# Optimization experiments

Measured on AMD Instinct MI355X. Metric: run time of the kernel, lower is better.

## Reference

```python
import jax, jax.numpy as jnp
import numpy as np

N = 100000      # nodes
E = 1600000     # edges (avg degree 16)
F_IN = 128      # node feature dim
HID = 128       # conv1 out
EMB = 64        # conv2 out (embedding)
OUT = 40        # classes


def setup_inputs() -> dict:
    key = jax.random.key(0)
    ks = jax.random.split(key, 8)
    x = jax.random.normal(ks[0], (N, F_IN), dtype=jnp.float32)
    edge_index = jax.random.randint(ks[1], (2, E), 0, N, dtype=jnp.int64)

    def glorot(k, shape):
        lim = np.sqrt(6.0 / (shape[0] + shape[1])).astype(np.float32)
        return jax.random.uniform(k, shape, jnp.float32, -lim, lim)

    W1 = glorot(ks[2], (F_IN, HID)); b1 = jnp.zeros((HID,), jnp.float32)
    W2 = glorot(ks[3], (HID, EMB)); b2 = jnp.zeros((EMB,), jnp.float32)
    Wl = glorot(ks[4], (EMB, OUT)); bl = jnp.zeros((OUT,), jnp.float32)
    return {"x": x, "edge_index": edge_index,
            "W1": W1, "b1": b1, "W2": W2, "b2": b2, "Wl": Wl, "bl": bl}


def _gcn_conv(x, W, b, src, dst, norm, n):
    # GCNConv: linear transform first (smaller width earlier), then normalized
    # sparse aggregation: out_i = sum_{j->i} norm_e * (x_j W) + b
    h = x @ W
    out = jax.ops.segment_sum(h[src] * norm[:, None], dst, num_segments=n)
    return out + b


def reference(x, edge_index, W1, b1, W2, b2, Wl, bl):
    n = x.shape[0]
    loop = jnp.arange(n, dtype=edge_index.dtype)
    # add self loops (GCNConv default)
    src = jnp.concatenate([edge_index[0], loop])
    dst = jnp.concatenate([edge_index[1], loop])
    # symmetric degree normalization: D^{-1/2} (A+I) D^{-1/2}
    deg = jax.ops.segment_sum(jnp.ones_like(dst, x.dtype), dst, num_segments=n)
    dinv = jnp.where(deg > 0, jax.lax.rsqrt(deg), 0.0)
    norm = dinv[src] * dinv[dst]

    h = jax.nn.relu(_gcn_conv(x, W1, b1, src, dst, norm, n))
    # F.dropout(training=False) is identity in eval mode
    embedding = _gcn_conv(h, W2, b2, src, dst, norm, n)
    logits = embedding @ Wl + bl
    return jax.nn.log_softmax(logits, axis=1), embedding
```

## Files before the change

### kernel.cpp

```cpp
#include <hip/hip_runtime.h>
#include <math.h>

#define F_IN 128
#define HIDN 128
#define EMBD 64
#define OUTC 40

#define NBINS 1024
#define BIN_SHIFT 7
#define CSR_BLKS 256

__host__ __device__ static inline int imin(int a, int b) { return a < b ? a : b; }

typedef __attribute__((ext_vector_type(8))) short s16x8;
typedef __attribute__((ext_vector_type(4))) float f32x4;

__device__ __forceinline__ unsigned short f2bf(float f) {
    unsigned int u = __builtin_bit_cast(unsigned int, f);
    u = (u + 0x7FFFu + ((u >> 16) & 1u)) >> 16;
    return (unsigned short)u;
}
__device__ __forceinline__ float bflo(unsigned int v) {
    return __builtin_bit_cast(float, v << 16);
}
__device__ __forceinline__ float bfhi(unsigned int v) {
    return __builtin_bit_cast(float, v & 0xFFFF0000u);
}

__host__ __device__ static inline int csr_chunk(int E) {
    return (((E + CSR_BLKS - 1) / CSR_BLKS) + 3) & ~3;
}


__global__ __launch_bounds__(256) void coarse_hist_kernel(const int* __restrict__ dst,
                                                          int* __restrict__ bc, int E) {
    __shared__ int h[NBINS];
    for (int i = threadIdx.x; i < NBINS; i += 256) h[i] = 0;
    __syncthreads();
    const int chunk = csr_chunk(E);
    const int e0 = blockIdx.x * chunk;
    const int e1 = imin(e0 + chunk, E);
    for (int e = e0 + threadIdx.x; e < e1; e += 256)
        atomicAdd(&h[dst[e] >> BIN_SHIFT], 1);
    __syncthreads();
    for (int i = threadIdx.x; i < NBINS; i += 256)
        bc[blockIdx.x * NBINS + i] = h[i];
}

__global__ __launch_bounds__(64) void bin_prefix_kernel(int* __restrict__ bc,
                                                        int* __restrict__ bintot) {
    const int bin = blockIdx.x * 64 + threadIdx.x;
    int run = 0;
    for (int blk = 0; blk < CSR_BLKS; ++blk) {
        int v = bc[blk * NBINS + bin];
        bc[blk * NBINS + bin] = run;
        run += v;
    }
    bintot[bin] = run;
}

__global__ __launch_bounds__(1024) void bin_scan_kernel(const int* __restrict__ bintot,
                                                        int* __restrict__ cs) {
    __shared__ int s[NBINS];
    const int t = threadIdx.x;
    s[t] = bintot[t];
    __syncthreads();
    for (int off = 1; off < NBINS; off <<= 1) {
        int v = (t >= off) ? s[t - off] : 0;
        __syncthreads();
        s[t] += v;
        __syncthreads();
    }
    cs[t + 1] = s[t];
    if (t == 0) cs[0] = 0;
}

__global__ __launch_bounds__(256) void bin_scatter_kernel(const int* __restrict__ src,
                                                          const int* __restrict__ dst,
                                                          const int* __restrict__ bc,
                                                          const int* __restrict__ cs,
                                                          int* __restrict__ ebuf, int E) {
    __shared__ int cur[NBINS];
    for (int i = threadIdx.x; i < NBINS; i += 256)
        cur[i] = cs[i] + bc[blockIdx.x * NBINS + i];
    __syncthreads();
    const int chunk = csr_chunk(E);
    const int e0 = blockIdx.x * chunk;
    const int e1 = imin(e0 + chunk, E);
    int e = e0 + threadIdx.x * 4;
    for (; e + 3 < e1; e += 256 * 4) {
        int4 d = *(const int4*)(dst + e);
        int4 s = *(const int4*)(src + e);
        int p0 = atomicAdd(&cur[d.x >> BIN_SHIFT], 1);
        int p1 = atomicAdd(&cur[d.y >> BIN_SHIFT], 1);
        int p2 = atomicAdd(&cur[d.z >> BIN_SHIFT], 1);
        int p3 = atomicAdd(&cur[d.w >> BIN_SHIFT], 1);
        ebuf[p0] = (s.x << BIN_SHIFT) | (d.x & 127);
        ebuf[p1] = (s.y << BIN_SHIFT) | (d.y & 127);
        ebuf[p2] = (s.z << BIN_SHIFT) | (d.z & 127);
        ebuf[p3] = (s.w << BIN_SHIFT) | (d.w & 127);
    }
    for (; e < e1; ++e) {
        int d = dst[e];
        int pos = atomicAdd(&cur[d >> BIN_SHIFT], 1);
        ebuf[pos] = (src[e] << BIN_SHIFT) | (d & 127);
    }
}

__global__ __launch_bounds__(256) void fine_build_kernel(const int* __restrict__ ebuf,
                                                         const int* __restrict__ cs,
                                                         int* __restrict__ degi,
                                                         int* __restrict__ rowptr,
                                                         float* __restrict__ dinv,
                                                         int* __restrict__ col, int n) {
    __shared__ int h[128];
    __shared__ int fs[128];
    __shared__ int cur[128];
    const int b = blockIdx.x;
    const int node0 = b << BIN_SHIFT;
    const int t = threadIdx.x;
    if (t < 128) h[t] = 0;
    __syncthreads();
    const int e0 = cs[b], e1 = cs[b + 1];
    for (int e = e0 + t; e < e1; e += 256)
        atomicAdd(&h[ebuf[e] & 127], 1);
    __syncthreads();
    if (t < 128) fs[t] = h[t];
    __syncthreads();
    for (int off = 1; off < 128; off <<= 1) {
        int v = 0;
        if (t < 128 && t >= off) v = fs[t - off];
        __syncthreads();
        if (t < 128) fs[t] += v;
        __syncthreads();
    }
    if (t < 128) {
        int node = node0 + t;
        if (node < n) {
            int cnt = h[t];
            degi[node] = cnt;
            rowptr[node] = e0 + fs[t] - cnt;
            dinv[node] = rsqrtf((float)cnt + 1.0f);
        }
        cur[t] = 0;
    }
    __syncthreads();
    for (int e = e0 + t; e < e1; e += 256) {
        int p = ebuf[e];
        int li = p & 127;
        int loc = atomicAdd(&cur[li], 1);
        col[e0 + (fs[li] - h[li]) + loc] = p >> BIN_SHIFT;
    }
}

template <typename InT, int K, int M, int WM, int WN>
__global__ __launch_bounds__(256) void gemm_mfma_kernel(const InT* __restrict__ X,
                                                        const float* __restrict__ W,
                                                        const float* __restrict__ dinv,
                                                        unsigned short* __restrict__ Y,
                                                        int n, int ntiles) {
    constexpr int BM = 64;
    constexpr int WR = BM / WM;
    constexpr int WC = M / WN;
    constexpr int RF = WR / 16;
    constexpr int CF = WC / 16;
    constexpr int KS = K / 32;
    constexpr int ROWB = K * 2;
    constexpr int UPR = ROWB / 16;

    __shared__ char Xs[BM * ROWB];

    const int tid = threadIdx.x;
    const int lane = tid & 63;
    const int wid = tid >> 6;
    const int wrow = wid / WN;
    const int wcol = wid % WN;
    const int l15 = lane & 15;
    const int lhi = lane >> 4;

    s16x8 bfrag[CF][KS];
#pragma unroll
    for (int cf = 0; cf < CF; ++cf)
#pragma unroll
        for (int ks = 0; ks < KS; ++ks) {
            const int colg = wcol * WC + cf * 16 + l15;
            const int kbase = ks * 32 + lhi * 8;
            s16x8 b;
#pragma unroll
            for (int j = 0; j < 8; ++j)
                b[j] = (short)f2bf(W[(size_t)(kbase + j) * M + colg]);
            bfrag[cf][ks] = b;
        }

    for (int tile = blockIdx.x; tile < ntiles; tile += gridDim.x) {
        const int row0 = tile * BM;
        __syncthreads();
#pragma unroll
        for (int i = 0; i < (BM * UPR) / 256; ++i) {
            int g = i * 256 + tid;
            int r = g / UPR, u = g % UPR;
            int grow = row0 + r;
            int4 val = make_int4(0, 0, 0, 0);
            if (grow < n) {
                if constexpr (sizeof(InT) == 4) {
                    const float* src = (const float*)X + (size_t)grow * K + u * 8;
                    float4 f0 = *(const float4*)src;
                    float4 f1 = *(const float4*)(src + 4);
                    val.x = (int)(f2bf(f0.x) | ((unsigned int)f2bf(f0.y) << 16));
                    val.y = (int)(f2bf(f0.z) | ((unsigned int)f2bf(f0.w) << 16));
                    val.z = (int)(f2bf(f1.x) | ((unsigned int)f2bf(f1.y) << 16));
                    val.w = (int)(f2bf(f1.z) | ((unsigned int)f2bf(f1.w) << 16));
                } else {
                    val = *(const int4*)((const unsigned short*)X + (size_t)grow * K + u * 8);
                }
            }
            *(int4*)(Xs + r * ROWB + ((u ^ (r & 7)) * 16)) = val;
        }
        __syncthreads();

        f32x4 acc[RF][CF];
#pragma unroll
        for (int rf = 0; rf < RF; ++rf)
#pragma unroll
            for (int cf = 0; cf < CF; ++cf) acc[rf][cf] = (f32x4)(0.0f);
#pragma unroll
        for (int ks = 0; ks < KS; ++ks) {
            s16x8 afrag[RF];
#pragma unroll
            for (int rf = 0; rf < RF; ++rf) {
                int r = wrow * WR + rf * 16 + l15;
                int u = ks * 4 + lhi;
                afrag[rf] = *(const s16x8*)(Xs + r * ROWB + ((u ^ (r & 7)) * 16));
            }
#pragma unroll
            for (int rf = 0; rf < RF; ++rf)
#pragma unroll
                for (int cf = 0; cf < CF; ++cf)
                    acc[rf][cf] = __builtin_amdgcn_mfma_f32_16x16x32_bf16(
                        afrag[rf], bfrag[cf][ks], acc[rf][cf], 0, 0, 0);
        }

#pragma unroll
        for (int rf = 0; rf < RF; ++rf) {
#pragma unroll
            for (int reg = 0; reg < 4; ++reg) {
                int grow = row0 + wrow * WR + rf * 16 + lhi * 4 + reg;
                if (grow < n) {
                    float dv = dinv[grow];
#pragma unroll
                    for (int cf = 0; cf < CF; ++cf) {
                        int colg = wcol * WC + cf * 16 + l15;
                        Y[(size_t)grow * M + colg] = f2bf(acc[rf][cf][reg] * dv);
                    }
                }
            }
        }
    }
}

__global__ __launch_bounds__(256) void gather_gemm_kernel(
    const unsigned short* __restrict__ Hs1, const int* __restrict__ rowptr,
    const int* __restrict__ degi, const int* __restrict__ col,
    const float* __restrict__ dinv, const float* __restrict__ b1,
    const float* __restrict__ W2, unsigned short* __restrict__ Hs2, int n) {
    __shared__ char h_tile[16 * 256];

    const int tid = threadIdx.x;
    const int lane = tid & 63;
    const int wv = tid >> 6;
    const int sub = lane & 15;
    const int grp = lane >> 4;
    const int node0 = blockIdx.x * 16;
    const int local = wv * 4 + grp;
    const int node = node0 + local;
    const int foff = sub * 8;

    s16x8 bfrag[4];
#pragma unroll
    for (int ks = 0; ks < 4; ++ks) {
        const int colg = wv * 16 + sub;
        const int kbase = ks * 32 + grp * 8;
        s16x8 bb;
#pragma unroll
        for (int j = 0; j < 8; ++j)
            bb[j] = (short)f2bf(W2[(size_t)(kbase + j) * EMBD + colg]);
        bfrag[ks] = bb;
    }

    if (node < n) {
        const int start = rowptr[node];
        const int cnt = degi[node];
        const float dvn = dinv[node];
        float acc[8];
        {
            int4 v = *(const int4*)(Hs1 + (size_t)node * HIDN + foff);
#pragma unroll
            for (int q = 0; q < 4; ++q) {
                unsigned int w = ((const unsigned int*)&v)[q];
                acc[2 * q] = bflo(w);
                acc[2 * q + 1] = bfhi(w);
            }
        }
        int m0 = imin(cnt, 16);
        int sv = (sub < m0) ? col[start + sub] : 0;
        for (int base = 0; base < cnt; base += 16) {
            int m = imin(cnt - base, 16);
            int svn = 0;
            int nb = base + 16;
            if (nb < cnt) {
                int mn = imin(cnt - nb, 16);
                svn = (sub < mn) ? col[start + nb + sub] : 0;
            }
            int k = 0;
            for (; k + 8 <= m; k += 8) {
                int4 a[8];
#pragma unroll
                for (int j = 0; j < 8; ++j) {
                    int s = __shfl(sv, k + j, 16);
                    a[j] = *(const int4*)(Hs1 + (size_t)s * HIDN + foff);
                }
#pragma unroll
                for (int j = 0; j < 8; ++j)
#pragma unroll
                    for (int q = 0; q < 4; ++q) {
                        unsigned int w = ((const unsigned int*)&a[j])[q];
                        acc[2 * q] += bflo(w);
                        acc[2 * q + 1] += bfhi(w);
                    }
            }
            for (; k + 2 <= m; k += 2) {
                int s0 = __shfl(sv, k, 16);
                int s1 = __shfl(sv, k + 1, 16);
                int4 a0 = *(const int4*)(Hs1 + (size_t)s0 * HIDN + foff);
                int4 a1 = *(const int4*)(Hs1 + (size_t)s1 * HIDN + foff);
#pragma unroll
                for (int q = 0; q < 4; ++q) {
                    unsigned int w0 = ((const unsigned int*)&a0)[q];
                    unsigned int w1 = ((const unsigned int*)&a1)[q];
                    acc[2 * q] += bflo(w0);
                    acc[2 * q + 1] += bfhi(w0);
                    acc[2 * q] += bflo(w1);
                    acc[2 * q + 1] += bfhi(w1);
                }
            }
            for (; k < m; ++k) {
                int s = __shfl(sv, k, 16);
                int4 a = *(const int4*)(Hs1 + (size_t)s * HIDN + foff);
#pragma unroll
                for (int q = 0; q < 4; ++q) {
                    unsigned int w = ((const unsigned int*)&a)[q];
                    acc[2 * q] += bflo(w);
                    acc[2 * q + 1] += bfhi(w);
                }
            }
            sv = svn;
        }
        float4 bv0 = *(const float4*)(b1 + foff);
        float4 bv1 = *(const float4*)(b1 + foff + 4);
        float o[8];
        o[0] = fmaxf(dvn * acc[0] + bv0.x, 0.f);
        o[1] = fmaxf(dvn * acc[1] + bv0.y, 0.f);
        o[2] = fmaxf(dvn * acc[2] + bv0.z, 0.f);
        o[3] = fmaxf(dvn * acc[3] + bv0.w, 0.f);
        o[4] = fmaxf(dvn * acc[4] + bv1.x, 0.f);
        o[5] = fmaxf(dvn * acc[5] + bv1.y, 0.f);
        o[6] = fmaxf(dvn * acc[6] + bv1.z, 0.f);
        o[7] = fmaxf(dvn * acc[7] + bv1.w, 0.f);
        int4 p;
        ((unsigned int*)&p)[0] = f2bf(o[0]) | ((unsigned int)f2bf(o[1]) << 16);
        ((unsigned int*)&p)[1] = f2bf(o[2]) | ((unsigned int)f2bf(o[3]) << 16);
        ((unsigned int*)&p)[2] = f2bf(o[4]) | ((unsigned int)f2bf(o[5]) << 16);
        ((unsigned int*)&p)[3] = f2bf(o[6]) | ((unsigned int)f2bf(o[7]) << 16);
        *(int4*)(h_tile + local * 256 + ((sub ^ (local & 7)) * 16)) = p;
    }
    __syncthreads();

    f32x4 acc2 = (f32x4)(0.0f);
#pragma unroll
    for (int ks = 0; ks < 4; ++ks) {
        int r = sub;
        int u = ks * 4 + grp;
        s16x8 af = *(const s16x8*)(h_tile + r * 256 + ((u ^ (r & 7)) * 16));
        acc2 = __builtin_amdgcn_mfma_f32_16x16x32_bf16(af, bfrag[ks], acc2, 0, 0, 0);
    }
#pragma unroll
    for (int reg = 0; reg < 4; ++reg) {
        int row = grp * 4 + reg;
        int nd = node0 + row;
        if (nd < n)
            Hs2[(size_t)nd * EMBD + wv * 16 + sub] = f2bf(acc2[reg] * dinv[nd]);
    }
}

template <int F, bool RELU, bool OBF>
__global__ __launch_bounds__(256) void gather_kernel(const unsigned short* __restrict__ Hs,
                                                     const int* __restrict__ rowptr,
                                                     const int* __restrict__ degi,
                                                     const int* __restrict__ col,
                                                     const float* __restrict__ dinv,
                                                     const float* __restrict__ b,
                                                     float* __restrict__ outf,
                                                     unsigned short* __restrict__ outb,
                                                     int n) {
    constexpr int LPF = F / 8;
    constexpr int NPW = 64 / LPF;
    const int lane = threadIdx.x & 63;
    const int wv = threadIdx.x >> 6;
    const int sub = lane & (LPF - 1);
    const int grp = lane / LPF;
    const int node = (blockIdx.x * 4 + wv) * NPW + grp;
    if (node >= n) return;
    const int start = rowptr[node];
    const int cnt = degi[node];
    const int foff = sub * 8;
    const float dvn = dinv[node];

    float acc[8];
    {
        int4 v = *(const int4*)(Hs + (size_t)node * F + foff);
#pragma unroll
        for (int q = 0; q < 4; ++q) {
            unsigned int w = ((const unsigned int*)&v)[q];
            acc[2 * q] = bflo(w);
            acc[2 * q + 1] = bfhi(w);
        }
    }

    int m0 = imin(cnt, LPF);
    int sv = (sub < m0) ? col[start + sub] : 0;
    for (int base = 0; base < cnt; base += LPF) {
        int m = imin(cnt - base, LPF);
        int svn = 0;
        int nb = base + LPF;
        if (nb < cnt) {
            int mn = imin(cnt - nb, LPF);
            svn = (sub < mn) ? col[start + nb + sub] : 0;
        }
        int k = 0;
        for (; k + 8 <= m; k += 8) {
            int4 a[8];
#pragma unroll
            for (int j = 0; j < 8; ++j) {
                int s = __shfl(sv, k + j, LPF);
                a[j] = *(const int4*)(Hs + (size_t)s * F + foff);
            }
#pragma unroll
            for (int j = 0; j < 8; ++j)
#pragma unroll
                for (int q = 0; q < 4; ++q) {
                    unsigned int w = ((const unsigned int*)&a[j])[q];
                    acc[2 * q] += bflo(w);
                    acc[2 * q + 1] += bfhi(w);
                }
        }
        for (; k < m; ++k) {
            int s = __shfl(sv, k, LPF);
            int4 a = *(const int4*)(Hs + (size_t)s * F + foff);
#pragma unroll
            for (int q = 0; q < 4; ++q) {
                unsigned int w = ((const unsigned int*)&a)[q];
                acc[2 * q] += bflo(w);
                acc[2 * q + 1] += bfhi(w);
            }
        }
        sv = svn;
    }

    float4 bv0 = *(const float4*)(b + foff);
    float4 bv1 = *(const float4*)(b + foff + 4);
    float o[8];
    o[0] = dvn * acc[0] + bv0.x; o[1] = dvn * acc[1] + bv0.y;
    o[2] = dvn * acc[2] + bv0.z; o[3] = dvn * acc[3] + bv0.w;
    o[4] = dvn * acc[4] + bv1.x; o[5] = dvn * acc[5] + bv1.y;
    o[6] = dvn * acc[6] + bv1.z; o[7] = dvn * acc[7] + bv1.w;
    if (RELU) {
#pragma unroll
        for (int j = 0; j < 8; ++j) o[j] = fmaxf(o[j], 0.0f);
    }
    if constexpr (OBF) {
        int4 p;
        ((unsigned int*)&p)[0] = f2bf(o[0]) | ((unsigned int)f2bf(o[1]) << 16);
        ((unsigned int*)&p)[1] = f2bf(o[2]) | ((unsigned int)f2bf(o[3]) << 16);
        ((unsigned int*)&p)[2] = f2bf(o[4]) | ((unsigned int)f2bf(o[5]) << 16);
        ((unsigned int*)&p)[3] = f2bf(o[6]) | ((unsigned int)f2bf(o[7]) << 16);
        *(int4*)(outb + (size_t)node * F + foff) = p;
    } else {
        float4 w0 = make_float4(o[0], o[1], o[2], o[3]);
        float4 w1 = make_float4(o[4], o[5], o[6], o[7]);
        *(float4*)(outf + (size_t)node * F + foff) = w0;
        *(float4*)(outf + (size_t)node * F + foff + 4) = w1;
    }
}

#define LSM_STRIDE 257
__global__ __launch_bounds__(256) void logits_lsm_kernel(const float* __restrict__ emb,
                                                         const float* __restrict__ Wl,
                                                         const float* __restrict__ bl,
                                                         float* __restrict__ out, int n) {
    __shared__ float Sbuf[EMBD * LSM_STRIDE];
    __shared__ float Wls[EMBD * OUTC];
    __shared__ float bls[OUTC];
    const int tid = threadIdx.x;
    const int node0 = blockIdx.x * 256;
    for (int i = tid; i < EMBD * OUTC; i += 256) Wls[i] = Wl[i];
    if (tid < OUTC) bls[tid] = bl[tid];

    const size_t base = (size_t)node0 * EMBD;
    const size_t total_elems = (size_t)n * EMBD;
    for (int it = 0; it < 16; ++it) {
        int idx = (tid + it * 256) * 4;
        int r = idx / EMBD, f = idx % EMBD;
        float4 v = make_float4(0.f, 0.f, 0.f, 0.f);
        if (base + idx + 3 < total_elems) v = *(const float4*)(emb + base + idx);
        Sbuf[(f + 0) * LSM_STRIDE + r] = v.x;
        Sbuf[(f + 1) * LSM_STRIDE + r] = v.y;
        Sbuf[(f + 2) * LSM_STRIDE + r] = v.z;
        Sbuf[(f + 3) * LSM_STRIDE + r] = v.w;
    }
    __syncthreads();

    float logit[OUTC];
#pragma unroll
    for (int o = 0; o < OUTC; ++o) logit[o] = bls[o];
    for (int f = 0; f < EMBD; ++f) {
        float ef = Sbuf[f * LSM_STRIDE + tid];
#pragma unroll
        for (int o = 0; o < OUTC; ++o) logit[o] = fmaf(ef, Wls[f * OUTC + o], logit[o]);
    }
    float mx = -INFINITY;
#pragma unroll
    for (int o = 0; o < OUTC; ++o) mx = fmaxf(mx, logit[o]);
    float s = 0.0f;
#pragma unroll
    for (int o = 0; o < OUTC; ++o) s += expf(logit[o] - mx);
    float lse = mx + logf(s);
    __syncthreads();
#pragma unroll
    for (int o = 0; o < OUTC; ++o) Sbuf[o * LSM_STRIDE + tid] = logit[o] - lse;
    __syncthreads();

    const size_t obase = (size_t)node0 * OUTC;
    const size_t ototal = (size_t)n * OUTC;
    for (int idx = tid; idx < 256 * OUTC; idx += 256) {
        size_t g = obase + idx;
        if (g < ototal) out[g] = Sbuf[(idx % OUTC) * LSM_STRIDE + (idx / OUTC)];
    }
}

extern "C" void kernel_launch(void* const* d_in, const int* in_sizes, int n_in,
                              void* d_out, int out_size, void* d_ws, size_t ws_size,
                              hipStream_t stream) {
    const float* x  = (const float*)d_in[0];
    const int*   ei = (const int*)d_in[1];
    const float* W1 = (const float*)d_in[2];
    const float* b1 = (const float*)d_in[3];
    const float* W2 = (const float*)d_in[4];
    const float* b2 = (const float*)d_in[5];
    const float* Wl = (const float*)d_in[6];
    const float* bl = (const float*)d_in[7];

    const int N = in_sizes[0] / F_IN;
    const int E = in_sizes[1] / 2;
    const int* srcp = ei;
    const int* dstp = ei + E;

    float* out = (float*)d_out;
    float* lsm = out;
    float* emb = out + (size_t)N * OUTC;

    float* ws    = (float*)d_ws;
    float* dinv  = ws;
    int*   degi  = (int*)(ws + N);
    int*   rowptr= degi + N;
    int*   cs    = rowptr + N;
    int*   bintot= cs + 1056;
    int*   bc    = bintot + NBINS;
    int*   col   = bc + CSR_BLKS * NBINS;
    int*   ebuf  = col + E;
    unsigned short* Hs1 = (unsigned short*)(ebuf + E);
    unsigned short* Hs2 = Hs1 + (size_t)N * HIDN;

    const int B = 256;
    const int ntiles = (N + 63) / 64;

    coarse_hist_kernel<<<CSR_BLKS, B, 0, stream>>>(dstp, bc, E);
    bin_prefix_kernel<<<NBINS / 64, 64, 0, stream>>>(bc, bintot);
    bin_scan_kernel<<<1, 1024, 0, stream>>>(bintot, cs);
    bin_scatter_kernel<<<CSR_BLKS, B, 0, stream>>>(srcp, dstp, bc, cs, ebuf, E);
    fine_build_kernel<<<(N + 127) / 128, B, 0, stream>>>(ebuf, cs, degi, rowptr, dinv, col, N);

    gemm_mfma_kernel<float, F_IN, HIDN, 2, 2><<<784, B, 0, stream>>>(x, W1, dinv, Hs1, N, ntiles);

    gather_gemm_kernel<<<(N + 15) / 16, B, 0, stream>>>(
        Hs1, rowptr, degi, col, dinv, b1, W2, Hs2, N);

    gather_kernel<EMBD, false, false><<<(N + 31) / 32, B, 0, stream>>>(
        Hs2, rowptr, degi, col, dinv, b2, emb, nullptr, N);

    logits_lsm_kernel<<<(N + 255) / 256, B, 0, stream>>>(emb, Wl, bl, lsm, N);
}
```

Baseline: 214.6 us.

## Fuse second aggregation with logits/log-softmax via MFMA and precompute weight fragments

```diff
diff --git a/kernel.cpp b/kernel.cpp
--- a/kernel.cpp
+++ b/kernel.cpp
@@ -31,6 +31,40 @@
     return (((E + CSR_BLKS - 1) / CSR_BLKS) + 3) & ~3;
 }
 
+__global__ __launch_bounds__(256) void prep_frags_kernel(
+    const float* __restrict__ W1, const float* __restrict__ W2,
+    const float* __restrict__ Wl, unsigned short* __restrict__ W1f,
+    unsigned short* __restrict__ W2f, unsigned short* __restrict__ Wlf) {
+    int s = blockIdx.x * 256 + threadIdx.x;
+    if (s < 2048) {
+        int lane = s & 63, r = s >> 6;
+        int ks = r & 3, cf = (r >> 2) & 3, wcol = r >> 4;
+        int c = wcol * 64 + cf * 16 + (lane & 15);
+        int kb = ks * 32 + (lane >> 4) * 8;
+        unsigned short* d = W1f + s * 8;
+#pragma unroll
+        for (int j = 0; j < 8; ++j) d[j] = f2bf(W1[(size_t)(kb + j) * HIDN + c]);
+    } else if (s < 3072) {
+        int q = s - 2048;
+        int lane = q & 63, r = q >> 6;
+        int ks = r & 3, wv = r >> 2;
+        int c = wv * 16 + (lane & 15);
+        int kb = ks * 32 + (lane >> 4) * 8;
+        unsigned short* d = W2f + q * 8;
+#pragma unroll
+        for (int j = 0; j < 8; ++j) d[j] = f2bf(W2[(size_t)(kb + j) * EMBD + c]);
+    } else if (s < 3456) {
+        int q = s - 3072;
+        int lane = q & 63, r = q >> 6;
+        int ks = r & 1, ct = r >> 1;
+        int c = ct * 16 + (lane & 15);
+        int kb = ks * 32 + (lane >> 4) * 8;
+        unsigned short* d = Wlf + q * 8;
+#pragma unroll
+        for (int j = 0; j < 8; ++j)
+            d[j] = (c < OUTC) ? f2bf(Wl[(size_t)(kb + j) * OUTC + c]) : (unsigned short)0;
+    }
+}
 
 __global__ __launch_bounds__(256) void coarse_hist_kernel(const int* __restrict__ dst,
                                                           int* __restrict__ bc, int E) {
@@ -155,7 +189,7 @@
 
 template <typename InT, int K, int M, int WM, int WN>
 __global__ __launch_bounds__(256) void gemm_mfma_kernel(const InT* __restrict__ X,
-                                                        const float* __restrict__ W,
+                                                        const unsigned short* __restrict__ Wfrag,
                                                         const float* __restrict__ dinv,
                                                         unsigned short* __restrict__ Y,
                                                         int n, int ntiles) {
@@ -182,15 +216,9 @@
 #pragma unroll
     for (int cf = 0; cf < CF; ++cf)
 #pragma unroll
-        for (int ks = 0; ks < KS; ++ks) {
-            const int colg = wcol * WC + cf * 16 + l15;
-            const int kbase = ks * 32 + lhi * 8;
-            s16x8 b;
-#pragma unroll
-            for (int j = 0; j < 8; ++j)
-                b[j] = (short)f2bf(W[(size_t)(kbase + j) * M + colg]);
-            bfrag[cf][ks] = b;
-        }
+        for (int ks = 0; ks < KS; ++ks)
+            bfrag[cf][ks] = *(const s16x8*)(Wfrag +
+                (size_t)(((wcol * CF + cf) * KS + ks) * 64 + lane) * 8);
 
     for (int tile = blockIdx.x; tile < ntiles; tile += gridDim.x) {
         const int row0 = tile * BM;
@@ -262,7 +290,7 @@
     const unsigned short* __restrict__ Hs1, const int* __restrict__ rowptr,
     const int* __restrict__ degi, const int* __restrict__ col,
     const float* __restrict__ dinv, const float* __restrict__ b1,
-    const float* __restrict__ W2, unsigned short* __restrict__ Hs2, int n) {
+    const unsigned short* __restrict__ W2f, unsigned short* __restrict__ Hs2, int n) {
     __shared__ char h_tile[16 * 256];
 
     const int tid = threadIdx.x;
@@ -277,15 +305,8 @@
 
     s16x8 bfrag[4];
 #pragma unroll
-    for (int ks = 0; ks < 4; ++ks) {
-        const int colg = wv * 16 + sub;
-        const int kbase = ks * 32 + grp * 8;
-        s16x8 bb;
-#pragma unroll
-        for (int j = 0; j < 8; ++j)
-            bb[j] = (short)f2bf(W2[(size_t)(kbase + j) * EMBD + colg]);
-        bfrag[ks] = bb;
-    }
+    for (int ks = 0; ks < 4; ++ks)
+        bfrag[ks] = *(const s16x8*)(W2f + (size_t)((wv * 4 + ks) * 64 + lane) * 8);
 
     if (node < n) {
         const int start = rowptr[node];
@@ -392,158 +413,141 @@
     }
 }
 
-template <int F, bool RELU, bool OBF>
-__global__ __launch_bounds__(256) void gather_kernel(const unsigned short* __restrict__ Hs,
-                                                     const int* __restrict__ rowptr,
-                                                     const int* __restrict__ degi,
-                                                     const int* __restrict__ col,
-                                                     const float* __restrict__ dinv,
-                                                     const float* __restrict__ b,
-                                                     float* __restrict__ outf,
-                                                     unsigned short* __restrict__ outb,
-                                                     int n) {
-    constexpr int LPF = F / 8;
-    constexpr int NPW = 64 / LPF;
-    const int lane = threadIdx.x & 63;
-    const int wv = threadIdx.x >> 6;
-    const int sub = lane & (LPF - 1);
-    const int grp = lane / LPF;
-    const int node = (blockIdx.x * 4 + wv) * NPW + grp;
-    if (node >= n) return;
-    const int start = rowptr[node];
-    const int cnt = degi[node];
+__global__ __launch_bounds__(256) void gather2_lsm_kernel(
+    const unsigned short* __restrict__ Hs, const int* __restrict__ rowptr,
+    const int* __restrict__ degi, const int* __restrict__ col,
+    const float* __restrict__ dinv, const float* __restrict__ b2,
+    const unsigned short* __restrict__ Wlf, const float* __restrict__ bl,
+    float* __restrict__ emb, float* __restrict__ lsm, int n) {
+    __shared__ char h_tile[32 * 128];
+    __shared__ float lg[32][49];
+    __shared__ float bls[OUTC];
+
+    const int tid = threadIdx.x;
+    if (tid < OUTC) bls[tid] = bl[tid];
+    const int lane = tid & 63;
+    const int wv = tid >> 6;
+    const int sub = lane & 7;
+    const int grp = lane >> 3;
+    const int local = wv * 8 + grp;
+    const int node0 = blockIdx.x * 32;
+    const int node = node0 + local;
     const int foff = sub * 8;
-    const float dvn = dinv[node];
-
-    float acc[8];
-    {
-        int4 v = *(const int4*)(Hs + (size_t)node * F + foff);
-#pragma unroll
-        for (int q = 0; q < 4; ++q) {
-            unsigned int w = ((const unsigned int*)&v)[q];
-            acc[2 * q] = bflo(w);
-            acc[2 * q + 1] = bfhi(w);
-        }
-    }
-
-    int m0 = imin(cnt, LPF);
-    int sv = (sub < m0) ? col[start + sub] : 0;
-    for (int base = 0; base < cnt; base += LPF) {
-        int m = imin(cnt - base, LPF);
-        int svn = 0;
-        int nb = base + LPF;
-        if (nb < cnt) {
-            int mn = imin(cnt - nb, LPF);
-            svn = (sub < mn) ? col[start + nb + sub] : 0;
-        }
-        int k = 0;
-        for (; k + 8 <= m; k += 8) {
-            int4 a[8];
-#pragma unroll
-            for (int j = 0; j < 8; ++j) {
-                int s = __shfl(sv, k + j, LPF);
-                a[j] = *(const int4*)(Hs + (size_t)s * F + foff);
-            }
-#pragma unroll
-            for (int j = 0; j < 8; ++j)
+
+    if (node < n) {
+        const int start = rowptr[node];
+        const int cnt = degi[node];
+        const float dvn = dinv[node];
+        float acc[8];
+        {
+            int4 v = *(const int4*)(Hs + (size_t)node * EMBD + foff);
+#pragma unroll
+            for (int q = 0; q < 4; ++q) {
+                unsigned int w = ((const unsigned int*)&v)[q];
+                acc[2 * q] = bflo(w);
+                acc[2 * q + 1] = bfhi(w);
+            }
+        }
+        int m0 = imin(cnt, 8);
+        int sv = (sub < m0) ? col[start + sub] : 0;
+        for (int base = 0; base < cnt; base += 8) {
+            int m = imin(cnt - base, 8);
+            int svn = 0;
+            int nb = base + 8;
+            if (nb < cnt) {
+                int mn = imin(cnt - nb, 8);
+                svn = (sub < mn) ? col[start + nb + sub] : 0;
+            }
+            int k = 0;
+            for (; k + 8 <= m; k += 8) {
+                int4 a[8];
+#pragma unroll
+                for (int j = 0; j < 8; ++j) {
+                    int s = __shfl(sv, k + j, 8);
+                    a[j] = *(const int4*)(Hs + (size_t)s * EMBD + foff);
+                }
+#pragma unroll
+                for (int j = 0; j < 8; ++j)
+#pragma unroll
+                    for (int q = 0; q < 4; ++q) {
+                        unsigned int w = ((const unsigned int*)&a[j])[q];
+                        acc[2 * q] += bflo(w);
+                        acc[2 * q + 1] += bfhi(w);
+                    }
+            }
+            for (; k < m; ++k) {
+                int s = __shfl(sv, k, 8);
+                int4 a = *(const int4*)(Hs + (size_t)s * EMBD + foff);
 #pragma unroll
                 for (int q = 0; q < 4; ++q) {
-                    unsigned int w = ((const unsigned int*)&a[j])[q];
+                    unsigned int w = ((const unsigned int*)&a)[q];
                     acc[2 * q] += bflo(w);
                     acc[2 * q + 1] += bfhi(w);
                 }
-        }
-        for (; k < m; ++k) {
-            int s = __shfl(sv, k, LPF);
-            int4 a = *(const int4*)(Hs + (size_t)s * F + foff);
-#pragma unroll
-            for (int q = 0; q < 4; ++q) {
-                unsigned int w = ((const unsigned int*)&a)[q];
-                acc[2 * q] += bflo(w);
-                acc[2 * q + 1] += bfhi(w);
-            }
-        }
-        sv = svn;
-    }
-
-    float4 bv0 = *(const float4*)(b + foff);
-    float4 bv1 = *(const float4*)(b + foff + 4);
-    float o[8];
-    o[0] = dvn * acc[0] + bv0.x; o[1] = dvn * acc[1] + bv0.y;
-    o[2] = dvn * acc[2] + bv0.z; o[3] = dvn * acc[3] + bv0.w;
-    o[4] = dvn * acc[4] + bv1.x; o[5] = dvn * acc[5] + bv1.y;
-    o[6] = dvn * acc[6] + bv1.z; o[7] = dvn * acc[7] + bv1.w;
-    if (RELU) {
-#pragma unroll
-        for (int j = 0; j < 8; ++j) o[j] = fmaxf(o[j], 0.0f);
-    }
-    if constexpr (OBF) {
+            }
+            sv = svn;
+        }
+
+        float4 bv0 = *(const float4*)(b2 + foff);
+        float4 bv1 = *(const float4*)(b2 + foff + 4);
+        float o[8];
+        o[0] = dvn * acc[0] + bv0.x; o[1] = dvn * acc[1] + bv0.y;
+        o[2] = dvn * acc[2] + bv0.z; o[3] = dvn * acc[3] + bv0.w;
+        o[4] = dvn * acc[4] + bv1.x; o[5] = dvn * acc[5] + bv1.y;
+        o[6] = dvn * acc[6] + bv1.z; o[7] = dvn * acc[7] + bv1.w;
+        *(float4*)(emb + (size_t)node * EMBD + foff) = make_float4(o[0], o[1], o[2], o[3]);
+        *(float4*)(emb + (size_t)node * EMBD + foff + 4) = make_float4(o[4], o[5], o[6], o[7]);
         int4 p;
         ((unsigned int*)&p)[0] = f2bf(o[0]) | ((unsigned int)f2bf(o[1]) << 16);
         ((unsigned int*)&p)[1] = f2bf(o[2]) | ((unsigned int)f2bf(o[3]) << 16);
         ((unsigned int*)&p)[2] = f2bf(o[4]) | ((unsigned int)f2bf(o[5]) << 16);
         ((unsigned int*)&p)[3] = f2bf(o[6]) | ((unsigned int)f2bf(o[7]) << 16);
-        *(int4*)(outb + (size_t)node * F + foff) = p;
-    } else {
-        float4 w0 = make_float4(o[0], o[1], o[2], o[3]);
-        float4 w1 = make_float4(o[4], o[5], o[6], o[7]);
-        *(float4*)(outf + (size_t)node * F + foff) = w0;
-        *(float4*)(outf + (size_t)node * F + foff + 4) = w1;
-    }
-}
-
-#define LSM_STRIDE 257
-__global__ __launch_bounds__(256) void logits_lsm_kernel(const float* __restrict__ emb,
-                                                         const float* __restrict__ Wl,
-                                                         const float* __restrict__ bl,
-                                                         float* __restrict__ out, int n) {
-    __shared__ float Sbuf[EMBD * LSM_STRIDE];
-    __shared__ float Wls[EMBD * OUTC];
-    __shared__ float bls[OUTC];
-    const int tid = threadIdx.x;
-    const int node0 = blockIdx.x * 256;
-    for (int i = tid; i < EMBD * OUTC; i += 256) Wls[i] = Wl[i];
-    if (tid < OUTC) bls[tid] = bl[tid];
-
-    const size_t base = (size_t)node0 * EMBD;
-    const size_t total_elems = (size_t)n * EMBD;
-    for (int it = 0; it < 16; ++it) {
-        int idx = (tid + it * 256) * 4;
-        int r = idx / EMBD, f = idx % EMBD;
-        float4 v = make_float4(0.f, 0.f, 0.f, 0.f);
-        if (base + idx + 3 < total_elems) v = *(const float4*)(emb + base + idx);
-        Sbuf[(f + 0) * LSM_STRIDE + r] = v.x;
-        Sbuf[(f + 1) * LSM_STRIDE + r] = v.y;
-        Sbuf[(f + 2) * LSM_STRIDE + r] = v.z;
-        Sbuf[(f + 3) * LSM_STRIDE + r] = v.w;
-    }
-    __syncthreads();
-
-    float logit[OUTC];
-#pragma unroll
-    for (int o = 0; o < OUTC; ++o) logit[o] = bls[o];
-    for (int f = 0; f < EMBD; ++f) {
-        float ef = Sbuf[f * LSM_STRIDE + tid];
-#pragma unroll
-        for (int o = 0; o < OUTC; ++o) logit[o] = fmaf(ef, Wls[f * OUTC + o], logit[o]);
-    }
-    float mx = -INFINITY;
-#pragma unroll
-    for (int o = 0; o < OUTC; ++o) mx = fmaxf(mx, logit[o]);
-    float s = 0.0f;
-#pragma unroll
-    for (int o = 0; o < OUTC; ++o) s += expf(logit[o] - mx);
-    float lse = mx + logf(s);
-    __syncthreads();
-#pragma unroll
-    for (int o = 0; o < OUTC; ++o) Sbuf[o * LSM_STRIDE + tid] = logit[o] - lse;
-    __syncthreads();
-
-    const size_t obase = (size_t)node0 * OUTC;
-    const size_t ototal = (size_t)n * OUTC;
-    for (int idx = tid; idx < 256 * OUTC; idx += 256) {
-        size_t g = obase + idx;
-        if (g < ototal) out[g] = Sbuf[(idx % OUTC) * LSM_STRIDE + (idx / OUTC)];
+        *(int4*)(h_tile + local * 128 + ((sub ^ (local & 7)) * 16)) = p;
+    }
+    __syncthreads();
+
+    const int l15 = lane & 15;
+    const int lhi = lane >> 4;
+#pragma unroll
+    for (int it = 0; it < 2; ++it) {
+        int t = wv + it * 4;
+        if (t < 6) {
+            int rt = t & 1, ct = t >> 1;
+            f32x4 accl = (f32x4)(0.0f);
+#pragma unroll
+            for (int ks = 0; ks < 2; ++ks) {
+                int r = rt * 16 + l15;
+                int u = ks * 4 + lhi;
+                s16x8 af = *(const s16x8*)(h_tile + r * 128 + ((u ^ (r & 7)) * 16));
+                s16x8 bf = *(const s16x8*)(Wlf + (size_t)((ct * 2 + ks) * 64 + lane) * 8);
+                accl = __builtin_amdgcn_mfma_f32_16x16x32_bf16(af, bf, accl, 0, 0, 0);
+            }
+#pragma unroll
+            for (int reg = 0; reg < 4; ++reg)
+                lg[rt * 16 + lhi * 4 + reg][ct * 16 + l15] = accl[reg];
+        }
+    }
+    __syncthreads();
+
+    if (tid < 32) {
+        int nd = node0 + tid;
+        if (nd < n) {
+            float logit[OUTC];
+            float mx = -INFINITY;
+#pragma unroll
+            for (int c = 0; c < OUTC; ++c) {
+                float v = lg[tid][c] + bls[c];
+                logit[c] = v;
+                mx = fmaxf(mx, v);
+            }
+            float ss = 0.0f;
+#pragma unroll
+            for (int c = 0; c < OUTC; ++c) ss += expf(logit[c] - mx);
+            float lse = mx + logf(ss);
+            float* op = lsm + (size_t)nd * OUTC;
+#pragma unroll
+            for (int c = 0; c < OUTC; ++c) op[c] = logit[c] - lse;
+        }
     }
 }
 
@@ -575,13 +579,18 @@
     int*   cs    = rowptr + N;
     int*   bintot= cs + 1056;
     int*   bc    = bintot + NBINS;
-    int*   col   = bc + CSR_BLKS * NBINS;
+    unsigned short* W1f = (unsigned short*)(bc + CSR_BLKS * NBINS);
+    unsigned short* W2f = W1f + 16384;
+    unsigned short* Wlf = W2f + 8192;
+    int*   col   = (int*)(Wlf + 3072);
     int*   ebuf  = col + E;
     unsigned short* Hs1 = (unsigned short*)(ebuf + E);
     unsigned short* Hs2 = Hs1 + (size_t)N * HIDN;
 
     const int B = 256;
     const int ntiles = (N + 63) / 64;
+
+    prep_frags_kernel<<<14, B, 0, stream>>>(W1, W2, Wl, W1f, W2f, Wlf);
 
     coarse_hist_kernel<<<CSR_BLKS, B, 0, stream>>>(dstp, bc, E);
     bin_prefix_kernel<<<NBINS / 64, 64, 0, stream>>>(bc, bintot);
@@ -589,13 +598,11 @@
     bin_scatter_kernel<<<CSR_BLKS, B, 0, stream>>>(srcp, dstp, bc, cs, ebuf, E);
     fine_build_kernel<<<(N + 127) / 128, B, 0, stream>>>(ebuf, cs, degi, rowptr, dinv, col, N);
 
-    gemm_mfma_kernel<float, F_IN, HIDN, 2, 2><<<784, B, 0, stream>>>(x, W1, dinv, Hs1, N, ntiles);
+    gemm_mfma_kernel<float, F_IN, HIDN, 2, 2><<<784, B, 0, stream>>>(x, W1f, dinv, Hs1, N, ntiles);
 
     gather_gemm_kernel<<<(N + 15) / 16, B, 0, stream>>>(
-        Hs1, rowptr, degi, col, dinv, b1, W2, Hs2, N);
-
-    gather_kernel<EMBD, false, false><<<(N + 31) / 32, B, 0, stream>>>(
-        Hs2, rowptr, degi, col, dinv, b2, emb, nullptr, N);
-
-    logits_lsm_kernel<<<(N + 255) / 256, B, 0, stream>>>(emb, Wl, bl, lsm, N);
-}
+        Hs1, rowptr, degi, col, dinv, b1, W2f, Hs2, N);
+
+    gather2_lsm_kernel<<<(N + 31) / 32, B, 0, stream>>>(
+        Hs2, rowptr, degi, col, dinv, b2, Wlf, bl, emb, lsm, N);
+}
```

Measured after the change: 190.9 us. 11.1% less time.
